# Kernel tuning notes

Hardware: AMD Instinct MI355X
Metric: run time of the kernel (lower is better)

## Reference

```python
import jax, jax.numpy as jnp
import numpy as np

B, N, D = 16, 1024, 768
SCALE = D ** (-0.5)


def setup_inputs() -> dict:
    key = jax.random.key(0)
    ks = jax.random.split(key, 6)
    return {
        "x": jax.random.normal(ks[0], (B, N, D), dtype=jnp.float32),
        "y": jax.random.normal(ks[1], (B, N, D), dtype=jnp.float32),
        "coords": jax.random.normal(ks[2], (N, N, 6), dtype=jnp.float32),
        "W_qk": jax.random.normal(ks[3], (D, D), dtype=jnp.float32) * (D ** -0.5),
        "pos_emb": jax.random.normal(ks[4], (N, 6, 1), dtype=jnp.float32) * 0.02,
        "gating": jnp.float32(1.0),
        "temp": jnp.float32(0.1),
    }


def reference(x, y, coords, W_qk, pos_emb, gating, temp):
    # k = Linear(y), no bias; torch Linear: y @ W.T
    k = jnp.einsum('bnd,ed->bne', y, W_qk)
    # content score [B, N, N]
    patch_score = jax.nn.softmax(jnp.einsum('bnd,bmd->bnm', x, k) * SCALE, axis=-1)
    # positional score: coords [N, N, 6] @ pos_emb [N, 6, 1] -> [N, N]
    pos_score = jax.nn.softmax(jnp.einsum('pnk,pkl->pnl', coords, pos_emb)[..., 0], axis=-1)
    g = jax.nn.sigmoid(gating)
    attn = (1.0 - g) * patch_score + g * pos_score[None, :, :]  # broadcast over B
    out = jnp.einsum('bnm,bmd->bnd', attn, y)
    entropy = jnp.sum(-attn * jnp.log(attn + 1e-8), axis=-1, keepdims=True)  # [B, N, 1]
    hmap = 2.0 * (1.0 - jax.nn.sigmoid(temp * entropy))
    return out, hmap
```

## Files before the change

kernel.cpp:

```cpp
#include <hip/hip_runtime.h>
#include <hip/hip_bf16.h>
#include <cstdint>

typedef __bf16 bf16_t;
typedef __bf16 bf16x8 __attribute__((ext_vector_type(8)));
typedef __bf16 bf16x4 __attribute__((ext_vector_type(4)));
typedef float f32x4 __attribute__((ext_vector_type(4)));

static constexpr int B = 16, N = 1024, D = 768;
static constexpr float SCALE = 0.03608439182435161f;

#define ASYNC_COPY16(gptr, lptr)                                                          \
  __builtin_amdgcn_global_load_lds((const __attribute__((address_space(1))) void*)(gptr), \
                                   (__attribute__((address_space(3))) void*)(lptr), 16, 0, 0)

__device__ __forceinline__ float wave_red_max(float v) {
#pragma unroll
  for (int o = 32; o > 0; o >>= 1) v = fmaxf(v, __shfl_down(v, o, 64));
  return v;
}
__device__ __forceinline__ float wave_red_sum(float v) {
#pragma unroll
  for (int o = 32; o > 0; o >>= 1) v += __shfl_down(v, o, 64);
  return v;
}
__device__ __forceinline__ float block_max(float v, float* sm) {
  v = wave_red_max(v);
  int lane = threadIdx.x & 63, w = threadIdx.x >> 6;
  if (lane == 0) sm[w] = v;
  __syncthreads();
  return fmaxf(fmaxf(sm[0], sm[1]), fmaxf(sm[2], sm[3]));
}
__device__ __forceinline__ float block_sum(float v, float* sm) {
  v = wave_red_sum(v);
  int lane = threadIdx.x & 63, w = threadIdx.x >> 6;
  if (lane == 0) sm[w] = v;
  __syncthreads();
  return sm[0] + sm[1] + sm[2] + sm[3];
}

__global__ __launch_bounds__(256) void cast_f32_bf16_4(const float4* __restrict__ in,
                                                       bf16x4* __restrict__ out, int n4) {
  int i = blockIdx.x * 256 + threadIdx.x;
  if (i < n4) {
    float4 v = in[i];
    bf16x4 o;
    o.x = (bf16_t)v.x; o.y = (bf16_t)v.y; o.z = (bf16_t)v.z; o.w = (bf16_t)v.w;
    out[i] = o;
  }
}

__global__ __launch_bounds__(256) void cast_transpose_y(const float* __restrict__ y,
                                                        bf16_t* __restrict__ yb,
                                                        bf16_t* __restrict__ yT) {
  __shared__ bf16_t t[32][33];
  int b = blockIdx.z;
  int d0 = blockIdx.x * 32;
  int n0 = blockIdx.y * 32;
  int tx = threadIdx.x & 31;
  int ty = threadIdx.x >> 5;
  const float* src = y + (size_t)b * N * D;
  bf16_t* dstN = yb + (size_t)b * N * D;
  bf16_t* dstT = yT + (size_t)b * N * D;
#pragma unroll
  for (int r = 0; r < 4; r++) {
    int n = n0 + ty + r * 8;
    float v = src[(size_t)n * D + d0 + tx];
    bf16_t h = (bf16_t)v;
    t[ty + r * 8][tx] = h;
    dstN[(size_t)n * D + d0 + tx] = h;
  }
  __syncthreads();
#pragma unroll
  for (int r = 0; r < 4; r++) {
    int d = d0 + ty + r * 8;
    dstT[(size_t)d * N + n0 + tx] = t[tx][ty + r * 8];
  }
}

__global__ __launch_bounds__(256) void pos_softmax_k(const float* __restrict__ coords,
                                                     const float* __restrict__ pemb,
                                                     float* __restrict__ pos) {
  __shared__ float sm1[4], sm2[4];
  int p = blockIdx.x;
  int tid = threadIdx.x;
  float e[6];
#pragma unroll
  for (int k = 0; k < 6; k++) e[k] = pemb[p * 6 + k];
  float v[4];
#pragma unroll
  for (int i = 0; i < 4; i++) {
    int n = tid + i * 256;
    const float* c = coords + ((size_t)p * N + n) * 6;
    float s = 0.f;
#pragma unroll
    for (int k = 0; k < 6; k++) s += c[k] * e[k];
    v[i] = s;
  }
  float m = block_max(fmaxf(fmaxf(v[0], v[1]), fmaxf(v[2], v[3])), sm1);
  float ex[4], ls = 0.f;
#pragma unroll
  for (int i = 0; i < 4; i++) { ex[i] = __expf(v[i] - m); ls += ex[i]; }
  float sum = block_sum(ls, sm2);
  float inv = 1.f / sum;
#pragma unroll
  for (int i = 0; i < 4; i++) pos[(size_t)p * N + tid + i * 256] = ex[i] * inv;
}

__global__ __launch_bounds__(256) void attn_entropy_k(float* __restrict__ S,
                                                      const float* __restrict__ pos,
                                                      const float* __restrict__ gating,
                                                      const float* __restrict__ temp,
                                                      float* __restrict__ hmap) {
  __shared__ float sm1[4], sm2[4], sm3[4];
  size_t row = blockIdx.x;
  int q = (int)(row & (size_t)(N - 1));
  int tid = threadIdx.x;
  float* Srow = S + row * N;
  float g = 1.f / (1.f + __expf(-gating[0]));
  float s[4];
#pragma unroll
  for (int i = 0; i < 4; i++) s[i] = Srow[tid + i * 256];
  float m = block_max(fmaxf(fmaxf(s[0], s[1]), fmaxf(s[2], s[3])), sm1);
  float e[4], ls = 0.f;
#pragma unroll
  for (int i = 0; i < 4; i++) { e[i] = __expf(s[i] - m); ls += e[i]; }
  float sum = block_sum(ls, sm2);
  float inv = 1.f / sum;
  const float* prow = pos + (size_t)q * N;
  float a[4], ent = 0.f;
#pragma unroll
  for (int i = 0; i < 4; i++) {
    float patch = e[i] * inv;
    float ps = prow[tid + i * 256];
    a[i] = (1.f - g) * patch + g * ps;
    ent += -a[i] * __logf(a[i] + 1e-8f);
  }
  float E = block_sum(ent, sm3);
  __syncthreads();
  bf16_t* arow = (bf16_t*)Srow;
#pragma unroll
  for (int i = 0; i < 4; i++) arow[tid + i * 256] = (bf16_t)a[i];
  if (tid == 0) hmap[row] = 2.f / (1.f + __expf(temp[0] * E));
}

template <typename OutT>
__global__ __launch_bounds__(512, 1) void gemm_nt_8p(const bf16_t* __restrict__ A, int lda, long long sA,
                                                     const bf16_t* __restrict__ Bm, int ldb, long long sB,
                                                     OutT* __restrict__ C, int ldc, long long sC,
                                                     int K, float scale, int swz) {
  __shared__ __align__(16) char lds_raw[131072];

  const int tid = threadIdx.x;
  const int lane = tid & 63, wave = tid >> 6;
  const int wr = wave >> 2, wc = wave & 3;
  const int quad = lane >> 4, lr = lane & 15;

  int bx = blockIdx.x, by = blockIdx.y, bz = blockIdx.z;
  if (swz) {
    int Gx = gridDim.x, Gy = gridDim.y, Gz = gridDim.z;
    int i = bx + Gx * (by + Gy * bz);
    int xcd = i & 7, slot = i >> 3;
    int T = Gx * Gy;
    int bpx = Gz >> 3;
    bz = xcd * bpx + slot / T;
    int t = slot % T;
    bx = t % Gx;
    by = t / Gx;
  }
  const int tileN = bx * 256, tileM = by * 256;
  A += (long long)bz * sA + (long long)tileM * lda;
  Bm += (long long)bz * sB + (long long)tileN * ldb;
  C += (long long)bz * sC;

  const int scol = (((tid & 7) ^ ((tid >> 3) & 7)) * 8);
  const bf16_t* a_src = A + (long long)(tid >> 3) * lda + scol;
  const bf16_t* b_src = Bm + (long long)(tid >> 3) * ldb + scol;

  auto STAGE_A = [&](int t, int h) {
    char* base = lds_raw + (t & 1) * 65536 + h * 16384 + wave * 1024;
    const bf16_t* g = a_src + (long long)(h * 128) * lda + t * 64;
    ASYNC_COPY16(g, base);
    ASYNC_COPY16(g + (long long)64 * lda, base + 8192);
  };
  auto STAGE_B = [&](int t, int h) {
    char* base = lds_raw + (t & 1) * 65536 + 32768 + h * 16384 + wave * 1024;
    const bf16_t* g = b_src + (long long)(h * 128) * ldb + t * 64;
    ASYNC_COPY16(g, base);
    ASYNC_COPY16(g + (long long)64 * ldb, base + 8192);
  };

  f32x4 acc[8][4];
#pragma unroll
  for (int i = 0; i < 8; i++)
#pragma unroll
    for (int j = 0; j < 4; j++) acc[i][j] = (f32x4){0.f, 0.f, 0.f, 0.f};

  const int nk = K >> 6;
  const int niter = nk >> 1;

  STAGE_A(0, 0); STAGE_A(0, 1); STAGE_B(0, 0); STAGE_B(0, 1);
  STAGE_B(1, 0); STAGE_B(1, 1);
  asm volatile("s_waitcnt vmcnt(4)" ::: "memory");
  __builtin_amdgcn_s_barrier();

  for (int it = 0; it < niter; ++it) {
    const int t1 = 2 * it + 1;
    const bool pf = (t1 + 1) < nk;
    bf16x8 bfr[4][2];
#pragma unroll
    for (int q = 0; q < 8; ++q) {
      const int hb = q >> 2, qq = q & 3;
      const bf16_t* As = (const bf16_t*)(lds_raw + hb * 65536 + wr * 16384);
      const bf16_t* Bs = (const bf16_t*)(lds_raw + hb * 65536 + 32768 + (wc >> 1) * 16384);
      if (qq == 0) {
#pragma unroll
        for (int nj = 0; nj < 4; ++nj)
#pragma unroll
          for (int kk = 0; kk < 2; ++kk)
            bfr[nj][kk] = *(const bf16x8*)&Bs[((wc & 1) * 64 + nj * 16 + lr) * 64 +
                                              ((kk * 32 + quad * 8) ^ ((lr & 7) * 8))];
      }
      bf16x8 af[2][2];
#pragma unroll
      for (int s = 0; s < 2; ++s)
#pragma unroll
        for (int kk = 0; kk < 2; ++kk)
          af[s][kk] = *(const bf16x8*)&As[((qq * 2 + s) * 16 + lr) * 64 +
                                          ((kk * 32 + quad * 8) ^ ((lr & 7) * 8))];
      if (q == 0) {
        STAGE_A(t1, 0);
      } else if (q == 1) {
        STAGE_A(t1, 1);
      } else if (q == 2) {
        if (pf) STAGE_B(t1 + 1, 0);
      } else if (q == 3) {
        if (pf) {
          STAGE_B(t1 + 1, 1);
          asm volatile("s_waitcnt vmcnt(4)" ::: "memory");
        } else {
          asm volatile("s_waitcnt vmcnt(0)" ::: "memory");
        }
      } else if (q == 4) {
        if (pf) STAGE_A(t1 + 1, 0);
      } else if (q == 5) {
        if (pf) STAGE_A(t1 + 1, 1);
      } else if (q == 6) {
        if (pf) STAGE_B(t1 + 2, 0);
      } else {
        if (pf) {
          STAGE_B(t1 + 2, 1);
          asm volatile("s_waitcnt vmcnt(4)" ::: "memory");
        }
      }
      __builtin_amdgcn_s_barrier();
      __builtin_amdgcn_s_setprio(1);
#pragma unroll
      for (int s = 0; s < 2; ++s)
#pragma unroll
        for (int nj = 0; nj < 4; ++nj)
#pragma unroll
          for (int kk = 0; kk < 2; ++kk)
            acc[qq * 2 + s][nj] =
                __builtin_amdgcn_mfma_f32_16x16x32_bf16(af[s][kk], bfr[nj][kk], acc[qq * 2 + s][nj], 0, 0, 0);
      __builtin_amdgcn_s_setprio(0);
      __builtin_amdgcn_s_barrier();
    }
  }
  __syncthreads();

  float* epi = (float*)lds_raw + wave * (16 * 68);
#pragma unroll
  for (int mi = 0; mi < 8; ++mi) {
#pragma unroll
    for (int nj = 0; nj < 4; ++nj)
#pragma unroll
      for (int r = 0; r < 4; ++r)
        epi[(quad * 4 + r) * 68 + nj * 16 + lr] = acc[mi][nj][r] * scale;
    if constexpr (sizeof(OutT) == 4) {
#pragma unroll
      for (int seg = 0; seg < 4; seg++) {
        int lrow = seg * 4 + (lane >> 4);
        f32x4 v = *(const f32x4*)&epi[lrow * 68 + (lane & 15) * 4];
        long long grow = tileM + wr * 128 + mi * 16 + lrow;
        int gcol = tileN + wc * 64 + (lane & 15) * 4;
        *(f32x4*)&C[grow * ldc + gcol] = v;
      }
    } else {
#pragma unroll
      for (int seg = 0; seg < 2; seg++) {
        int lrow = seg * 8 + (lane >> 3);
        const float* p = &epi[lrow * 68 + (lane & 7) * 8];
        f32x4 v0 = *(const f32x4*)&p[0];
        f32x4 v1 = *(const f32x4*)&p[4];
        bf16x8 o;
#pragma unroll
        for (int j = 0; j < 4; j++) { o[j] = (bf16_t)v0[j]; o[j + 4] = (bf16_t)v1[j]; }
        long long grow = tileM + wr * 128 + mi * 16 + lrow;
        int gcol = tileN + wc * 64 + (lane & 7) * 8;
        *(bf16x8*)&C[grow * ldc + gcol] = o;
      }
    }
  }
}

extern "C" void kernel_launch(void* const* d_in, const int* in_sizes, int n_in,
                              void* d_out, int out_size, void* d_ws, size_t ws_size,
                              hipStream_t stream) {
  const float* x = (const float*)d_in[0];
  const float* y = (const float*)d_in[1];
  const float* coords = (const float*)d_in[2];
  const float* W = (const float*)d_in[3];
  const float* pemb = (const float*)d_in[4];
  const float* gating = (const float*)d_in[5];
  const float* temp = (const float*)d_in[6];
  float* out = (float*)d_out;
  float* hmap = out + (size_t)B * N * D;

  char* ws = (char*)d_ws;
  bf16_t* xb = (bf16_t*)(ws + 0);
  bf16_t* yb = (bf16_t*)(ws + 25165824);
  bf16_t* yT = (bf16_t*)(ws + 50331648);
  bf16_t* Wb = (bf16_t*)(ws + 75497472);
  bf16_t* kb = (bf16_t*)(ws + 76677120);
  float* pos = (float*)(ws + 101842944);
  float* S   = (float*)(ws + 106037248);

  const int BND = B * N * D;

  cast_f32_bf16_4<<<BND / 4 / 256, 256, 0, stream>>>((const float4*)x, (bf16x4*)xb, BND / 4);
  cast_f32_bf16_4<<<(D * D / 4 + 255) / 256, 256, 0, stream>>>((const float4*)W, (bf16x4*)Wb, D * D / 4);
  cast_transpose_y<<<dim3(D / 32, N / 32, B), 256, 0, stream>>>(y, yb, yT);
  pos_softmax_k<<<N, 256, 0, stream>>>(coords, pemb, pos);

  gemm_nt_8p<bf16_t><<<dim3(D / 256, (B * N) / 256, 1), 512, 0, stream>>>(
      yb, D, 0LL, Wb, D, 0LL, kb, D, 0LL, D, 1.0f, 0);

  gemm_nt_8p<float><<<dim3(N / 256, N / 256, B), 512, 0, stream>>>(
      xb, D, (long long)N * D, kb, D, (long long)N * D, S, N, (long long)N * N, D, SCALE, 1);

  attn_entropy_k<<<B * N, 256, 0, stream>>>(S, pos, gating, temp, hmap);

  gemm_nt_8p<float><<<dim3(D / 256, N / 256, B), 512, 0, stream>>>(
      (const bf16_t*)S, 2 * N, (long long)N * 2 * N, yT, N, (long long)N * D, out, D, (long long)N * D, N, 1.0f, 1);
}
```

Measured before the change: 294.6 us.

## Reorder GEMM inner loop by k-half and drop one barrier per phase

Restructures the main GEMM loop so each phase handles one 32-wide k-slice over four m-rows instead of both k-slices over two m-rows. B fragments are loaded per k-half, which shrinks register use. The per-phase pre-MFMA barrier is removed and the vmcnt waits move after the MFMAs. The global-to-LDS staging slots are reshuffled to fit the new schedule. The intent is less synchronisation, fewer live registers and better overlap of loads with compute, at the risk of LDS hazards if the new wait counts are wrong.

```diff
diff --git a/kernel.cpp b/kernel.cpp
--- a/kernel.cpp
+++ b/kernel.cpp
@@ -207,63 +207,53 @@
   for (int it = 0; it < niter; ++it) {
     const int t1 = 2 * it + 1;
     const bool pf = (t1 + 1) < nk;
-    bf16x8 bfr[4][2];
+    bf16x8 bfr[4];
 #pragma unroll
     for (int q = 0; q < 8; ++q) {
       const int hb = q >> 2, qq = q & 3;
+      const int kk = qq >> 1, mh = qq & 1;
       const bf16_t* As = (const bf16_t*)(lds_raw + hb * 65536 + wr * 16384);
       const bf16_t* Bs = (const bf16_t*)(lds_raw + hb * 65536 + 32768 + (wc >> 1) * 16384);
-      if (qq == 0) {
-#pragma unroll
-        for (int nj = 0; nj < 4; ++nj)
-#pragma unroll
-          for (int kk = 0; kk < 2; ++kk)
-            bfr[nj][kk] = *(const bf16x8*)&Bs[((wc & 1) * 64 + nj * 16 + lr) * 64 +
-                                              ((kk * 32 + quad * 8) ^ ((lr & 7) * 8))];
-      }
-      bf16x8 af[2][2];
-#pragma unroll
-      for (int s = 0; s < 2; ++s)
-#pragma unroll
-        for (int kk = 0; kk < 2; ++kk)
-          af[s][kk] = *(const bf16x8*)&As[((qq * 2 + s) * 16 + lr) * 64 +
-                                          ((kk * 32 + quad * 8) ^ ((lr & 7) * 8))];
       if (q == 0) {
         STAGE_A(t1, 0);
       } else if (q == 1) {
         STAGE_A(t1, 1);
-      } else if (q == 2) {
+      } else if (q == 3) {
         if (pf) STAGE_B(t1 + 1, 0);
-      } else if (q == 3) {
-        if (pf) {
-          STAGE_B(t1 + 1, 1);
-          asm volatile("s_waitcnt vmcnt(4)" ::: "memory");
-        } else {
-          asm volatile("s_waitcnt vmcnt(0)" ::: "memory");
-        }
       } else if (q == 4) {
+        if (pf) STAGE_B(t1 + 1, 1);
+      } else if (q == 5) {
         if (pf) STAGE_A(t1 + 1, 0);
-      } else if (q == 5) {
+      } else if (q == 6) {
         if (pf) STAGE_A(t1 + 1, 1);
-      } else if (q == 6) {
-        if (pf) STAGE_B(t1 + 2, 0);
-      } else {
-        if (pf) {
-          STAGE_B(t1 + 2, 1);
-          asm volatile("s_waitcnt vmcnt(4)" ::: "memory");
-        }
-      }
-      __builtin_amdgcn_s_barrier();
+      } else if (q == 7) {
+        if (pf) { STAGE_B(t1 + 2, 0); STAGE_B(t1 + 2, 1); }
+      }
+      if (mh == 0) {
+#pragma unroll
+        for (int nj = 0; nj < 4; ++nj)
+          bfr[nj] = *(const bf16x8*)&Bs[((wc & 1) * 64 + nj * 16 + lr) * 64 +
+                                        ((kk * 32 + quad * 8) ^ ((lr & 7) * 8))];
+      }
+      bf16x8 af[4];
+#pragma unroll
+      for (int s = 0; s < 4; ++s)
+        af[s] = *(const bf16x8*)&As[((mh * 4 + s) * 16 + lr) * 64 +
+                                    ((kk * 32 + quad * 8) ^ ((lr & 7) * 8))];
       __builtin_amdgcn_s_setprio(1);
 #pragma unroll
-      for (int s = 0; s < 2; ++s)
+      for (int s = 0; s < 4; ++s)
 #pragma unroll
         for (int nj = 0; nj < 4; ++nj)
-#pragma unroll
-          for (int kk = 0; kk < 2; ++kk)
-            acc[qq * 2 + s][nj] =
-                __builtin_amdgcn_mfma_f32_16x16x32_bf16(af[s][kk], bfr[nj][kk], acc[qq * 2 + s][nj], 0, 0, 0);
+          acc[mh * 4 + s][nj] =
+              __builtin_amdgcn_mfma_f32_16x16x32_bf16(af[s], bfr[nj], acc[mh * 4 + s][nj], 0, 0, 0);
       __builtin_amdgcn_s_setprio(0);
+      if (q == 3) {
+        if (pf) asm volatile("s_waitcnt vmcnt(2)" ::: "memory");
+        else    asm volatile("s_waitcnt vmcnt(0)" ::: "memory");
+      } else if (q == 7) {
+        if (pf) asm volatile("s_waitcnt vmcnt(4)" ::: "memory");
+      }
       __builtin_amdgcn_s_barrier();
     }
   }
```

Result: slower. 300.8 us (+2.1%).
